# Performance work log

Hardware: AMD Instinct MI355X
Metric: run time of the kernel (lower is better)

The kernel has to match this reference:

```python
import jax, jax.numpy as jnp
import numpy as np

B, A, G = 2, 256, 65536  # batch, num_atoms (= sum(Z)), num_grid_points


def setup_inputs() -> dict:
    key = jax.random.key(0)
    k1, k2, k3 = jax.random.split(key, 3)
    R_tensor = jax.random.normal(k1, (B, A, 3), dtype=jnp.float32)
    coords = jax.random.normal(k2, (G, 3), dtype=jnp.float32)
    weight = jax.random.normal(k3, (3, 3), dtype=jnp.float32)  # 'exp_matrix' param
    Z = jnp.ones((A,), dtype=jnp.int32)  # atomic numbers; sum(Z) == A
    return {"R_tensor": R_tensor, "coords": coords, "weight": weight, "Z": Z}


def reference(R_tensor, coords, weight, Z):
    # diff[b, g, a, :] = coords[g] - R_tensor[b, a]   -> (B, G, A, 3)
    diff = coords[None, :, None, :] - R_tensor[:, None, :, :]
    # tf.einsum('ijkl,ml->ijkm', diff, weight): apply 3x3 transform on last axis
    t = jnp.einsum('bgal,ml->bgam', diff, weight)
    # Euclidean norm over last axis -> (B, G, A)
    d = jnp.sqrt(jnp.sum(t * t, axis=-1))
    # exp then reduce over atoms -> (B, G)
    return jnp.sum(jnp.exp(d), axis=2)
```

## Files before the change

### kernel.cpp

```cpp
#include <hip/hip_runtime.h>
#include <math.h>

#define NB 2
#define NA 256
#define NG 65536

#define LOG2E 1.4426950408889634074f

#if __has_builtin(__builtin_amdgcn_sqrtf)
#define FSQRT(x) __builtin_amdgcn_sqrtf(x)
#else
#define FSQRT(x) sqrtf(x)
#endif

#if __has_builtin(__builtin_amdgcn_exp2f)
#define FEXP2(x) __builtin_amdgcn_exp2f(x)
#else
#define FEXP2(x) __expf((x) * 0.69314718055994530942f)
#endif

__global__ __launch_bounds__(256) void init_layer_fused(
    const float* __restrict__ R,
    const float* __restrict__ coords,
    const float* __restrict__ W,
    float* __restrict__ out)
{
    __shared__ float4 sAtom[NA];
    __shared__ float  red[256];

    const int tid   = threadIdx.x;
    const int gl    = tid & 63;
    const int slice = __builtin_amdgcn_readfirstlane(tid >> 6);
    const int b     = blockIdx.y;
    const int g     = blockIdx.x * 64 + gl;

    const float w00 = W[0], w01 = W[1], w02 = W[2];
    const float w10 = W[3], w11 = W[4], w12 = W[5];
    const float w20 = W[6], w21 = W[7], w22 = W[8];

    {
        const int base = (b * NA + tid) * 3;
        const float rx = R[base + 0];
        const float ry = R[base + 1];
        const float rz = R[base + 2];
        const float sx = LOG2E * (w00 * rx + w01 * ry + w02 * rz);
        const float sy = LOG2E * (w10 * rx + w11 * ry + w12 * rz);
        const float sz = LOG2E * (w20 * rx + w21 * ry + w22 * rz);
        sAtom[tid] = make_float4(-2.0f * sx, -2.0f * sy, -2.0f * sz,
                                 sx * sx + sy * sy + sz * sz);
    }

    const float cx = coords[g * 3 + 0];
    const float cy = coords[g * 3 + 1];
    const float cz = coords[g * 3 + 2];
    const float tx = LOG2E * (w00 * cx + w01 * cy + w02 * cz);
    const float ty = LOG2E * (w10 * cx + w11 * cy + w12 * cz);
    const float tz = LOG2E * (w20 * cx + w21 * cy + w22 * cz);
    const float t2 = tx * tx + ty * ty + tz * tz;

    __syncthreads();

    const float4* __restrict__ wsb = sAtom + slice * 64;

    float s0 = 0.0f, s1 = 0.0f, s2 = 0.0f, s3 = 0.0f;

    #pragma unroll 4
    for (int a = 0; a < 64; a += 4) {
        const float4 p0 = wsb[a + 0];
        const float4 p1 = wsb[a + 1];
        const float4 p2 = wsb[a + 2];
        const float4 p3 = wsb[a + 3];

        const float d0 = fmaf(p0.x, tx, fmaf(p0.y, ty, fmaf(p0.z, tz, p0.w + t2)));
        const float d1 = fmaf(p1.x, tx, fmaf(p1.y, ty, fmaf(p1.z, tz, p1.w + t2)));
        const float d2 = fmaf(p2.x, tx, fmaf(p2.y, ty, fmaf(p2.z, tz, p2.w + t2)));
        const float d3 = fmaf(p3.x, tx, fmaf(p3.y, ty, fmaf(p3.z, tz, p3.w + t2)));

        s0 += FEXP2(FSQRT(fmaxf(d0, 0.0f)));
        s1 += FEXP2(FSQRT(fmaxf(d1, 0.0f)));
        s2 += FEXP2(FSQRT(fmaxf(d2, 0.0f)));
        s3 += FEXP2(FSQRT(fmaxf(d3, 0.0f)));
    }

    red[tid] = (s0 + s1) + (s2 + s3);
    __syncthreads();

    if (tid < 64) {
        out[b * NG + blockIdx.x * 64 + tid] =
            (red[tid] + red[tid + 64]) + (red[tid + 128] + red[tid + 192]);
    }
}

extern "C" void kernel_launch(void* const* d_in, const int* in_sizes, int n_in,
                              void* d_out, int out_size, void* d_ws, size_t ws_size,
                              hipStream_t stream) {
    const float* R      = (const float*)d_in[0];
    const float* coords = (const float*)d_in[1];
    const float* W      = (const float*)d_in[2];
    float* out = (float*)d_out;

    dim3 grid(NG / 64, NB);
    init_layer_fused<<<grid, dim3(256), 0, stream>>>(R, coords, W, out);
}
```

Baseline: 68.16 us.

## Process four grid points per thread to reuse LDS atom loads

```diff
diff --git a/kernel.cpp b/kernel.cpp
--- a/kernel.cpp
+++ b/kernel.cpp
@@ -4,6 +4,9 @@
 #define NB 2
 #define NA 256
 #define NG 65536
+
+#define GP   4
+#define GPB  (64 * GP)
 
 #define LOG2E 1.4426950408889634074f
 
@@ -26,17 +29,26 @@
     float* __restrict__ out)
 {
     __shared__ float4 sAtom[NA];
-    __shared__ float  red[256];
+    __shared__ float  red[4 * GPB];
 
     const int tid   = threadIdx.x;
-    const int gl    = tid & 63;
+    const int lane  = tid & 63;
     const int slice = __builtin_amdgcn_readfirstlane(tid >> 6);
     const int b     = blockIdx.y;
-    const int g     = blockIdx.x * 64 + gl;
+    const int gbase = blockIdx.x * GPB;
 
     const float w00 = W[0], w01 = W[1], w02 = W[2];
     const float w10 = W[3], w11 = W[4], w12 = W[5];
     const float w20 = W[6], w21 = W[7], w22 = W[8];
+
+    float cx[GP], cy[GP], cz[GP];
+    #pragma unroll
+    for (int p = 0; p < GP; ++p) {
+        const int g = gbase + p * 64 + lane;
+        cx[p] = coords[g * 3 + 0];
+        cy[p] = coords[g * 3 + 1];
+        cz[p] = coords[g * 3 + 2];
+    }
 
     {
         const int base = (b * NA + tid) * 3;
@@ -50,45 +62,51 @@
                                  sx * sx + sy * sy + sz * sz);
     }
 
-    const float cx = coords[g * 3 + 0];
-    const float cy = coords[g * 3 + 1];
-    const float cz = coords[g * 3 + 2];
-    const float tx = LOG2E * (w00 * cx + w01 * cy + w02 * cz);
-    const float ty = LOG2E * (w10 * cx + w11 * cy + w12 * cz);
-    const float tz = LOG2E * (w20 * cx + w21 * cy + w22 * cz);
-    const float t2 = tx * tx + ty * ty + tz * tz;
+    float tx[GP], ty[GP], tz[GP], t2[GP];
+    #pragma unroll
+    for (int p = 0; p < GP; ++p) {
+        tx[p] = LOG2E * (w00 * cx[p] + w01 * cy[p] + w02 * cz[p]);
+        ty[p] = LOG2E * (w10 * cx[p] + w11 * cy[p] + w12 * cz[p]);
+        tz[p] = LOG2E * (w20 * cx[p] + w21 * cy[p] + w22 * cz[p]);
+        t2[p] = tx[p] * tx[p] + ty[p] * ty[p] + tz[p] * tz[p];
+    }
 
     __syncthreads();
 
     const float4* __restrict__ wsb = sAtom + slice * 64;
 
-    float s0 = 0.0f, s1 = 0.0f, s2 = 0.0f, s3 = 0.0f;
+    float accA[GP], accB[GP];
+    #pragma unroll
+    for (int p = 0; p < GP; ++p) { accA[p] = 0.0f; accB[p] = 0.0f; }
 
-    #pragma unroll 4
     for (int a = 0; a < 64; a += 4) {
         const float4 p0 = wsb[a + 0];
         const float4 p1 = wsb[a + 1];
         const float4 p2 = wsb[a + 2];
         const float4 p3 = wsb[a + 3];
 
-        const float d0 = fmaf(p0.x, tx, fmaf(p0.y, ty, fmaf(p0.z, tz, p0.w + t2)));
-        const float d1 = fmaf(p1.x, tx, fmaf(p1.y, ty, fmaf(p1.z, tz, p1.w + t2)));
-        const float d2 = fmaf(p2.x, tx, fmaf(p2.y, ty, fmaf(p2.z, tz, p2.w + t2)));
-        const float d3 = fmaf(p3.x, tx, fmaf(p3.y, ty, fmaf(p3.z, tz, p3.w + t2)));
+        #pragma unroll
+        for (int p = 0; p < GP; ++p) {
+            const float d0 = fmaf(p0.x, tx[p], fmaf(p0.y, ty[p], fmaf(p0.z, tz[p], p0.w + t2[p])));
+            const float d1 = fmaf(p1.x, tx[p], fmaf(p1.y, ty[p], fmaf(p1.z, tz[p], p1.w + t2[p])));
+            const float d2 = fmaf(p2.x, tx[p], fmaf(p2.y, ty[p], fmaf(p2.z, tz[p], p2.w + t2[p])));
+            const float d3 = fmaf(p3.x, tx[p], fmaf(p3.y, ty[p], fmaf(p3.z, tz[p], p3.w + t2[p])));
 
-        s0 += FEXP2(FSQRT(fmaxf(d0, 0.0f)));
-        s1 += FEXP2(FSQRT(fmaxf(d1, 0.0f)));
-        s2 += FEXP2(FSQRT(fmaxf(d2, 0.0f)));
-        s3 += FEXP2(FSQRT(fmaxf(d3, 0.0f)));
+            accA[p] += FEXP2(FSQRT(fmaxf(d0, 0.0f)));
+            accB[p] += FEXP2(FSQRT(fmaxf(d1, 0.0f)));
+            accA[p] += FEXP2(FSQRT(fmaxf(d2, 0.0f)));
+            accB[p] += FEXP2(FSQRT(fmaxf(d3, 0.0f)));
+        }
     }
 
-    red[tid] = (s0 + s1) + (s2 + s3);
+    #pragma unroll
+    for (int p = 0; p < GP; ++p)
+        red[slice * GPB + p * 64 + lane] = accA[p] + accB[p];
+
     __syncthreads();
 
-    if (tid < 64) {
-        out[b * NG + blockIdx.x * 64 + tid] =
-            (red[tid] + red[tid + 64]) + (red[tid + 128] + red[tid + 192]);
-    }
+    out[b * NG + gbase + tid] =
+        (red[tid] + red[GPB + tid]) + (red[2 * GPB + tid] + red[3 * GPB + tid]);
 }
 
 extern "C" void kernel_launch(void* const* d_in, const int* in_sizes, int n_in,
@@ -99,6 +117,6 @@
     const float* W      = (const float*)d_in[2];
     float* out = (float*)d_out;
 
-    dim3 grid(NG / 64, NB);
+    dim3 grid(NG / GPB, NB);
     init_layer_fused<<<grid, dim3(256), 0, stream>>>(R, coords, W, out);
 }
```

New measurement: 67.43 us. About the same (-1.1%).
